# Kernel optimization log

Measured on AMD Instinct MI355X. Metric: run time of the kernel, lower is better.

The kernel has to match this reference:

```python
import jax, jax.numpy as jnp
import numpy as np

B, C = 2, 4
SPATIAL = (128, 128, 128)
N_PTS = 32          # num_points_per_class
THR = 0.5           # threshold


def setup_inputs() -> dict:
    key = jax.random.key(0)
    logits = jax.random.normal(key, (B, C) + SPATIAL, dtype=jnp.float32)
    return {"logits": logits}


def _extract_points(logits):
    """Vectorized equivalent of the per-(batch,class) nonzero/topk loop.

    For every (b, c): softmax prob > THR defines candidates; top-k by prob
    selects up to N_PTS points. Classes are visited in the original order
    (foreground 1..C-1, then background 0); valid points are compacted to
    the front per batch element; padding has label -1 and coords 0.
    Output width is fixed at C*N_PTS (jit-friendly) instead of the batch
    max count, but all valid (coord, label) entries and their order match.
    """
    b, c = logits.shape[:2]
    spatial = logits.shape[2:]
    dims = len(spatial)
    S = int(np.prod(spatial))
    probs = jax.nn.softmax(logits, axis=1).reshape(b, c, S)  # [b,c,S]
    # class visitation order: 1..C-1 then 0 (background last)
    order = jnp.concatenate([jnp.arange(1, c), jnp.arange(1)])  # [c]
    probs = probs[:, order]                                    # [b,c,S]
    score = jnp.where(probs > THR, probs, -jnp.inf)
    top_vals, top_idx = jax.lax.top_k(score, N_PTS)            # [b,c,N_PTS]
    valid = top_vals > -jnp.inf                                # [b,c,N_PTS]
    coords = jnp.stack(jnp.unravel_index(top_idx, spatial), axis=-1)  # [b,c,N_PTS,dims]
    labels = jnp.where(valid, order[None, :, None], -1)        # [b,c,N_PTS]
    coords = jnp.where(valid[..., None], coords, 0)
    # flatten classes and compact valid points to the front (stable sort)
    N = c * N_PTS
    labels = labels.reshape(b, N)
    coords = coords.reshape(b, N, dims)
    perm = jnp.argsort((labels < 0).astype(jnp.int32), axis=1, stable=True)  # [b,N]
    labels = jnp.take_along_axis(labels, perm, axis=1)
    coords = jnp.take_along_axis(coords, perm[..., None], axis=1)
    return coords.astype(jnp.int32), labels.astype(jnp.int32)


def reference(logits):
    coords, labels = _extract_points(logits)
    return coords, labels
```

## Files before the change

### kernel.cpp

```cpp
#include <hip/hip_runtime.h>
#include <stdint.h>

#define Bn 2
#define Cn 4
#define Sn (128 * 128 * 128)
#define NPTS 32
#define NBINS 1025
#define THRf 0.5f
#define PB 4096
#define BT 512
#define BT2 1024
#define FB 1024

typedef float f32x4 __attribute__((ext_vector_type(4)));

__device__ __forceinline__ int bin_of_bits(unsigned int u) {
    return (int)((u - 0x3F000000u) >> 13);
}

__device__ __forceinline__ void softmax_argmax4(float l0, float l1, float l2, float l3,
                                                int* cm_out, float* p_out) {
    float m = fmaxf(fmaxf(l0, l1), fmaxf(l2, l3));
    float e0 = expf(l0 - m);
    float e1 = expf(l1 - m);
    float e2 = expf(l2 - m);
    float e3 = expf(l3 - m);
    float s = ((e0 + e1) + e2) + e3;
    float em = e0; int cm = 0;
    if (e1 > em) { em = e1; cm = 1; }
    if (e2 > em) { em = e2; cm = 2; }
    if (e3 > em) { em = e3; cm = 3; }
    *cm_out = cm;
    *p_out = em / s;
}


__global__ __launch_bounds__(BT, 8) void fused_stream(const float* __restrict__ logits,
                                                      unsigned int* __restrict__ cnt,
                                                      unsigned int* __restrict__ gh,
                                                      uint2* __restrict__ cand,
                                                      int cap) {
    __shared__ unsigned int lh[Cn * NBINS];
    __shared__ unsigned int lcut[Cn], cls_cnt[Cn], cls_base[Cn], cls_pos[Cn];
    const int b = blockIdx.y;
    const int t = threadIdx.x;
    const int lane = t & 63;
    for (int j = t; j < Cn * NBINS; j += BT) lh[j] = 0u;
    if (t < Cn) { lcut[t] = 0u; cls_cnt[t] = 0u; cls_pos[t] = 0u; }
    __syncthreads();

    const float* base = logits + (size_t)b * Cn * Sn;
    const f32x4* s0 = (const f32x4*)base;
    const f32x4* s1 = (const f32x4*)(base + Sn);
    const f32x4* s2 = (const f32x4*)(base + 2 * Sn);
    const f32x4* s3 = (const f32x4*)(base + 3 * Sn);
    const int qs = blockIdx.x * (PB / 4);
    const int q0 = qs + t;
    const int q1 = qs + BT + t;
    f32x4 u0 = s0[q0], u1 = s1[q0], u2 = s2[q0], u3 = s3[q0];
    f32x4 w0 = s0[q1], w1 = s1[q1], w2 = s2[q1], w3 = s3[q1];
    __builtin_amdgcn_sched_barrier(0);

    unsigned int pk[PB / BT];
    #pragma unroll
    for (int k = 0; k < 4; ++k) {
        int cm; float p;
        softmax_argmax4(u0[k], u1[k], u2[k], u3[k], &cm, &p);
        unsigned int pv = 0u;
        if (p > THRf) {
            unsigned int off = __float_as_uint(p) - 0x3F000000u;
            atomicAdd(&lh[cm * NBINS + (int)(off >> 13)], 1u);
            pv = (off << 2) | (unsigned int)cm;
        }
        pk[k] = pv;
    }
    #pragma unroll
    for (int k = 0; k < 4; ++k) {
        int cm; float p;
        softmax_argmax4(w0[k], w1[k], w2[k], w3[k], &cm, &p);
        unsigned int pv = 0u;
        if (p > THRf) {
            unsigned int off = __float_as_uint(p) - 0x3F000000u;
            atomicAdd(&lh[cm * NBINS + (int)(off >> 13)], 1u);
            pv = (off << 2) | (unsigned int)cm;
        }
        pk[4 + k] = pv;
    }
    __syncthreads();

    {
        const int wave = t >> 6;
        if (wave < Cn) {
            const unsigned int* h = &lh[wave * NBINS];
            const int lo = lane * 17;
            unsigned int cs = 0;
            #pragma unroll
            for (int k = 0; k < 17; ++k) {
                int bin = lo + k;
                if (bin < NBINS) cs += h[bin];
            }
            unsigned int S = cs;
            #pragma unroll
            for (int off = 1; off < 64; off <<= 1) {
                unsigned int v = __shfl_down(S, off, 64);
                if (lane + off < 64) S += v;
            }
            unsigned int suf = S - cs;
            if (S >= NPTS && suf < NPTS) {
                unsigned int acc = suf;
                int hi = min(lo + 16, NBINS - 1);
                for (int bin = hi; bin >= lo; --bin) {
                    acc += h[bin];
                    if (acc >= NPTS) {
                        lcut[wave] = (unsigned int)bin;
                        cls_cnt[wave] = acc;
                        break;
                    }
                }
            }
            if (lane == 0 && S < NPTS) cls_cnt[wave] = S;
        }
    }
    __syncthreads();

    {
        const int wave = t >> 6;
        if (wave < Cn) {
            const unsigned int* h = &lh[wave * NBINS];
            unsigned int* g = gh + (size_t)(b * Cn + wave) * NBINS;
            for (int bin = (int)lcut[wave] + lane; bin < NBINS; bin += 64) {
                unsigned int v = h[bin];
                if (v) atomicAdd(&g[bin], v);
            }
        }
    }
    if (t < Cn && cls_cnt[t] > 0)
        cls_base[t] = atomicAdd(&cnt[b * Cn + t], cls_cnt[t]);
    __syncthreads();

    #pragma unroll
    for (int j = 0; j < PB / BT; ++j) {
        unsigned int pv = pk[j];
        if (pv != 0u) {
            unsigned int cm = pv & 3u;
            if ((pv >> 15) >= lcut[cm]) {
                unsigned int pos = cls_base[cm] + atomicAdd(&cls_pos[cm], 1u);
                if (pos < (unsigned int)cap) {
                    int it = j >> 2, k = j & 3;
                    unsigned int idx = (unsigned int)((qs + it * BT + t) * 4 + k);
                    cand[(size_t)(b * Cn + cm) * cap + pos] =
                        make_uint2(0x3F000000u + (pv >> 2), idx);
                }
            }
        }
    }
}

__global__ __launch_bounds__(BT2) void select_emit(const unsigned int* __restrict__ cnt,
                                                   const unsigned int* __restrict__ gh,
                                                   const uint2* __restrict__ cand,
                                                   int cap,
                                                   unsigned int* __restrict__ done,
                                                   unsigned int* __restrict__ validn,
                                                   uint2* __restrict__ topk,
                                                   int* __restrict__ out) {
    __shared__ unsigned int lh[NBINS];
    __shared__ uint2 fbuf[FB];
    __shared__ unsigned int s_T, s_m, s_old;
    __shared__ int pre[Cn + 1];
    const int bc = blockIdx.x, t = threadIdx.x;
    const int b = bc >> 2;
    const int lane = t & 63;

    for (int j = t; j < NBINS; j += BT2) lh[j] = gh[(size_t)bc * NBINS + j];
    if (t == 0) { s_T = 0u; s_m = 0u; }
    __syncthreads();
    const int n = min((int)cnt[bc], cap);

    if (t < 64) {
        const int lo = lane * 17;
        unsigned int cs = 0;
        #pragma unroll
        for (int k = 0; k < 17; ++k) {
            int bin = lo + k;
            if (bin < NBINS) cs += lh[bin];
        }
        unsigned int S = cs;
        #pragma unroll
        for (int off = 1; off < 64; off <<= 1) {
            unsigned int v = __shfl_down(S, off, 64);
            if (lane + off < 64) S += v;
        }
        unsigned int suf = S - cs;
        if (S >= NPTS && suf < NPTS) {
            unsigned int acc = suf;
            int hi = min(lo + 16, NBINS - 1);
            for (int bin = hi; bin >= lo; --bin) {
                acc += lh[bin];
                if (acc >= NPTS) { s_T = (unsigned int)bin; break; }
            }
        }
    }
    __syncthreads();
    const unsigned int T = s_T;

    {
        const uint2* src = cand + (size_t)bc * cap;
        for (int j0 = t; j0 < n; j0 += BT2 * 8) {
            uint2 e[8];
            #pragma unroll
            for (int k = 0; k < 8; ++k) {
                int j = j0 + k * BT2;
                e[k] = src[j < n ? j : (n > 0 ? n - 1 : 0)];
            }
            #pragma unroll
            for (int k = 0; k < 8; ++k) {
                int j = j0 + k * BT2;
                if (j < n && (unsigned int)bin_of_bits(e[k].x) >= T) {
                    unsigned int pos = atomicAdd(&s_m, 1u);
                    if (pos < FB) fbuf[pos] = e[k];
                }
            }
        }
    }
    __syncthreads();

    const int m = min((int)s_m, FB);
    const int vn = min(n, NPTS);
    if (t == 0) validn[bc] = (unsigned int)vn;
    for (int i = t; i < m; i += BT2) {
        uint2 e = fbuf[i];
        int rank = 0;
        for (int j = 0; j < m; ++j) {
            uint2 o = fbuf[j];
            rank += (int)((o.x > e.x) || (o.x == e.x && o.y < e.y));
        }
        if (rank < vn) topk[bc * NPTS + rank] = e;
    }

    __threadfence();
    __syncthreads();
    if (t == 0) s_old = atomicAdd(&done[b], 1u);
    __syncthreads();
    if (s_old != 3u) return;
    __threadfence();

    if (t == 0) {
        int acc = 0;
        for (int oc = 0; oc < Cn; ++oc) {
            pre[oc] = acc;
            acc += (int)validn[b * Cn + ((oc + 1) & 3)];
        }
        pre[Cn] = acc;
    }
    __syncthreads();

    if (t < Cn * NPTS) {
        const int j = t;
        int label = -1, z = 0, y = 0, x = 0;
        if (j < pre[Cn]) {
            int oc = 0;
            while (j >= pre[oc + 1]) ++oc;
            int c = (oc + 1) & 3;
            int r = j - pre[oc];
            uint2 e = topk[(b * Cn + c) * NPTS + r];
            int idx = (int)e.y;
            z = idx >> 14;
            y = (idx >> 7) & 127;
            x = idx & 127;
            label = c;
        }
        int* coords = out;
        int* labels = out + Bn * Cn * NPTS * 3;
        int bo = b * Cn * NPTS + j;
        coords[bo * 3 + 0] = z;
        coords[bo * 3 + 1] = y;
        coords[bo * 3 + 2] = x;
        labels[bo] = label;
    }
}

extern "C" void kernel_launch(void* const* d_in, const int* in_sizes, int n_in,
                              void* d_out, int out_size, void* d_ws, size_t ws_size,
                              hipStream_t stream) {
    const float* logits = (const float*)d_in[0];
    int* out = (int*)d_out;

    unsigned int* cnt = (unsigned int*)d_ws;
    unsigned int* done = cnt + Bn * Cn;
    unsigned int* gh = done + Bn;
    unsigned int* validn = gh + Bn * Cn * NBINS;
    uint2* topk = (uint2*)(validn + Bn * Cn);
    uint2* cand = topk + Bn * Cn * NPTS;
    size_t fixed = (size_t)((char*)cand - (char*)d_ws);
    int cap = (int)((ws_size - fixed) / (Bn * Cn * sizeof(uint2)));
    if (cap > (1 << 18)) cap = 1 << 18;
    if (cap < 4096) cap = 4096;

    hipMemsetAsync(cnt, 0, (size_t)(Bn * Cn + Bn + Bn * Cn * NBINS) * sizeof(unsigned int),
                   stream);

    dim3 grid(Sn / PB, Bn);
    fused_stream<<<grid, BT, 0, stream>>>(logits, cnt, gh, cand, cap);
    select_emit<<<Bn * Cn, BT2, 0, stream>>>(cnt, gh, cand, cap, done, validn, topk, out);
}
```

Baseline: 120.0 us.

## Prefilter voxels with fast exp sum and compact candidates into per-wave LDS queue

Computes a cheap softmax denominator with fast __expf and uses a conservative bound (sum < ~2) to decide whether the max probability can exceed the threshold. Only passing voxels are compacted via ballot/mbcnt into a per-wave shared-memory queue, and the full softmax/argmax and histogram atomics run densely on that queue. Overflow beyond the queue falls back to inline processing. The aim is to cut divergent exact-softmax and atomic work for the many voxels that cannot qualify, at the cost of extra LDS, dropping the occupancy hint from launch bounds, and a looser load schedule with two sequential load batches.

Result: no change. 119.6 us (-0.4%).

```diff
diff --git a/kernel.cpp b/kernel.cpp
--- a/kernel.cpp
+++ b/kernel.cpp
@@ -11,6 +11,7 @@
 #define BT 512
 #define BT2 1024
 #define FB 1024
+#define QW 128
 
 typedef float f32x4 __attribute__((ext_vector_type(4)));
 
@@ -35,16 +36,19 @@
 }
 
 
-__global__ __launch_bounds__(BT, 8) void fused_stream(const float* __restrict__ logits,
-                                                      unsigned int* __restrict__ cnt,
-                                                      unsigned int* __restrict__ gh,
-                                                      uint2* __restrict__ cand,
-                                                      int cap) {
+__global__ __launch_bounds__(BT) void fused_stream(const float* __restrict__ logits,
+                                                   unsigned int* __restrict__ cnt,
+                                                   unsigned int* __restrict__ gh,
+                                                   uint2* __restrict__ cand,
+                                                   int cap) {
     __shared__ unsigned int lh[Cn * NBINS];
+    __shared__ float4 qlog[8][QW];
+    __shared__ unsigned short qidx[8][QW];
     __shared__ unsigned int lcut[Cn], cls_cnt[Cn], cls_base[Cn], cls_pos[Cn];
     const int b = blockIdx.y;
     const int t = threadIdx.x;
     const int lane = t & 63;
+    const int wv = t >> 6;
     for (int j = t; j < Cn * NBINS; j += BT) lh[j] = 0u;
     if (t < Cn) { lcut[t] = 0u; cls_cnt[t] = 0u; cls_pos[t] = 0u; }
     __syncthreads();
@@ -55,43 +59,71 @@
     const f32x4* s2 = (const f32x4*)(base + 2 * Sn);
     const f32x4* s3 = (const f32x4*)(base + 3 * Sn);
     const int qs = blockIdx.x * (PB / 4);
-    const int q0 = qs + t;
-    const int q1 = qs + BT + t;
-    f32x4 u0 = s0[q0], u1 = s1[q0], u2 = s2[q0], u3 = s3[q0];
-    f32x4 w0 = s0[q1], w1 = s1[q1], w2 = s2[q1], w3 = s3[q1];
-    __builtin_amdgcn_sched_barrier(0);
-
-    unsigned int pk[PB / BT];
+
+    unsigned int pk[PB / BT] = {0u, 0u, 0u, 0u, 0u, 0u, 0u, 0u};
+    unsigned int wq = 0u;
     #pragma unroll
-    for (int k = 0; k < 4; ++k) {
+    for (int it = 0; it < PB / 4 / BT; ++it) {
+        int q = qs + it * BT + t;
+        f32x4 v0 = s0[q], v1 = s1[q], v2 = s2[q], v3 = s3[q];
+        #pragma unroll
+        for (int k = 0; k < 4; ++k) {
+            float l0 = v0[k], l1 = v1[k], l2 = v2[k], l3 = v3[k];
+            float m = fmaxf(fmaxf(l0, l1), fmaxf(l2, l3));
+            float st = ((__expf(l0 - m) + __expf(l1 - m)) + __expf(l2 - m))
+                       + __expf(l3 - m);
+            bool c = st < 2.0009766f;
+            unsigned long long mk = __ballot(c);
+            unsigned int nb = __builtin_amdgcn_mbcnt_lo((unsigned int)mk, 0u);
+            nb = __builtin_amdgcn_mbcnt_hi((unsigned int)(mk >> 32), nb);
+            unsigned int pos = wq + nb;
+            if (c) {
+                if (pos < QW) {
+                    qlog[wv][pos] = make_float4(l0, l1, l2, l3);
+                    qidx[wv][pos] = (unsigned short)((it * BT + t) * 4 + k);
+                } else {
+                    int cm; float p;
+                    softmax_argmax4(l0, l1, l2, l3, &cm, &p);
+                    if (p > THRf) {
+                        unsigned int off = __float_as_uint(p) - 0x3F000000u;
+                        atomicAdd(&lh[cm * NBINS + (int)(off >> 13)], 1u);
+                        pk[it * 4 + k] = (off << 2) | (unsigned int)cm;
+                    }
+                }
+            }
+            wq += (unsigned int)__popcll(mk);
+        }
+    }
+
+    const unsigned int nq = min(wq, (unsigned int)QW);
+    unsigned int spv0 = 0u, sidx0 = 0u, spv1 = 0u, sidx1 = 0u;
+    if ((unsigned int)lane < nq) {
+        float4 L = qlog[wv][lane];
         int cm; float p;
-        softmax_argmax4(u0[k], u1[k], u2[k], u3[k], &cm, &p);
-        unsigned int pv = 0u;
+        softmax_argmax4(L.x, L.y, L.z, L.w, &cm, &p);
         if (p > THRf) {
             unsigned int off = __float_as_uint(p) - 0x3F000000u;
             atomicAdd(&lh[cm * NBINS + (int)(off >> 13)], 1u);
-            pv = (off << 2) | (unsigned int)cm;
-        }
-        pk[k] = pv;
-    }
-    #pragma unroll
-    for (int k = 0; k < 4; ++k) {
+            spv0 = (off << 2) | (unsigned int)cm;
+            sidx0 = qidx[wv][lane];
+        }
+    }
+    if ((unsigned int)(64 + lane) < nq) {
+        float4 L = qlog[wv][64 + lane];
         int cm; float p;
-        softmax_argmax4(w0[k], w1[k], w2[k], w3[k], &cm, &p);
-        unsigned int pv = 0u;
+        softmax_argmax4(L.x, L.y, L.z, L.w, &cm, &p);
         if (p > THRf) {
             unsigned int off = __float_as_uint(p) - 0x3F000000u;
             atomicAdd(&lh[cm * NBINS + (int)(off >> 13)], 1u);
-            pv = (off << 2) | (unsigned int)cm;
-        }
-        pk[4 + k] = pv;
+            spv1 = (off << 2) | (unsigned int)cm;
+            sidx1 = qidx[wv][64 + lane];
+        }
     }
     __syncthreads();
 
     {
-        const int wave = t >> 6;
-        if (wave < Cn) {
-            const unsigned int* h = &lh[wave * NBINS];
+        if (wv < Cn) {
+            const unsigned int* h = &lh[wv * NBINS];
             const int lo = lane * 17;
             unsigned int cs = 0;
             #pragma unroll
@@ -112,23 +144,22 @@
                 for (int bin = hi; bin >= lo; --bin) {
                     acc += h[bin];
                     if (acc >= NPTS) {
-                        lcut[wave] = (unsigned int)bin;
-                        cls_cnt[wave] = acc;
+                        lcut[wv] = (unsigned int)bin;
+                        cls_cnt[wv] = acc;
                         break;
                     }
                 }
             }
-            if (lane == 0 && S < NPTS) cls_cnt[wave] = S;
+            if (lane == 0 && S < NPTS) cls_cnt[wv] = S;
         }
     }
     __syncthreads();
 
     {
-        const int wave = t >> 6;
-        if (wave < Cn) {
-            const unsigned int* h = &lh[wave * NBINS];
-            unsigned int* g = gh + (size_t)(b * Cn + wave) * NBINS;
-            for (int bin = (int)lcut[wave] + lane; bin < NBINS; bin += 64) {
+        if (wv < Cn) {
+            const unsigned int* h = &lh[wv * NBINS];
+            unsigned int* g = gh + (size_t)(b * Cn + wv) * NBINS;
+            for (int bin = (int)lcut[wv] + lane; bin < NBINS; bin += 64) {
                 unsigned int v = h[bin];
                 if (v) atomicAdd(&g[bin], v);
             }
@@ -138,18 +169,40 @@
         cls_base[t] = atomicAdd(&cnt[b * Cn + t], cls_cnt[t]);
     __syncthreads();
 
-    #pragma unroll
-    for (int j = 0; j < PB / BT; ++j) {
-        unsigned int pv = pk[j];
-        if (pv != 0u) {
-            unsigned int cm = pv & 3u;
-            if ((pv >> 15) >= lcut[cm]) {
+    {
+        if (spv0 != 0u) {
+            unsigned int cm = spv0 & 3u;
+            if ((spv0 >> 15) >= lcut[cm]) {
                 unsigned int pos = cls_base[cm] + atomicAdd(&cls_pos[cm], 1u);
-                if (pos < (unsigned int)cap) {
-                    int it = j >> 2, k = j & 3;
-                    unsigned int idx = (unsigned int)((qs + it * BT + t) * 4 + k);
+                if (pos < (unsigned int)cap)
                     cand[(size_t)(b * Cn + cm) * cap + pos] =
-                        make_uint2(0x3F000000u + (pv >> 2), idx);
+                        make_uint2(0x3F000000u + (spv0 >> 2),
+                                   (unsigned int)(qs * 4) + sidx0);
+            }
+        }
+        if (spv1 != 0u) {
+            unsigned int cm = spv1 & 3u;
+            if ((spv1 >> 15) >= lcut[cm]) {
+                unsigned int pos = cls_base[cm] + atomicAdd(&cls_pos[cm], 1u);
+                if (pos < (unsigned int)cap)
+                    cand[(size_t)(b * Cn + cm) * cap + pos] =
+                        make_uint2(0x3F000000u + (spv1 >> 2),
+                                   (unsigned int)(qs * 4) + sidx1);
+            }
+        }
+        #pragma unroll
+        for (int j = 0; j < PB / BT; ++j) {
+            unsigned int pv = pk[j];
+            if (pv != 0u) {
+                unsigned int cm = pv & 3u;
+                if ((pv >> 15) >= lcut[cm]) {
+                    unsigned int pos = cls_base[cm] + atomicAdd(&cls_pos[cm], 1u);
+                    if (pos < (unsigned int)cap) {
+                        unsigned int idx =
+                            (unsigned int)((qs + (j >> 2) * BT + t) * 4 + (j & 3));
+                        cand[(size_t)(b * Cn + cm) * cap + pos] =
+                            make_uint2(0x3F000000u + (pv >> 2), idx);
+                    }
                 }
             }
         }
```
